# Performance work log

Measured on AMD Instinct MI355X. Metric: run time of the kernel, lower is better.

## Reference

```python
import jax, jax.numpy as jnp
import numpy as np

B, F, H, E = 16, 128, 144, 24   # batch, frames, num_harmonies, embedding
C0, C1 = 12, 12                 # harmony component dims (root, quality)


def setup_inputs() -> dict:
    key = jax.random.key(0)
    ks = jax.random.split(key, 7)
    note_embedding_seq = jax.random.normal(ks[0], (B, F, E), jnp.float32)
    # one-hot harmony vectors: concat(one_hot(root), one_hot(quality))
    idx = np.arange(H)
    hv = np.zeros((H, E), np.float32)
    hv[idx, idx // C1] = 1.0
    hv[idx, C0 + idx % C1] = 1.0
    harmony_vector = jnp.asarray(np.broadcast_to(hv, (B, H, E)).copy())
    s = 1.0 / np.sqrt(E)
    W0 = jax.random.uniform(ks[1], (C0, C0), jnp.float32, -s, s)
    b0 = jax.random.uniform(ks[2], (C0,), jnp.float32, -s, s)
    W1 = jax.random.uniform(ks[3], (C1, C1), jnp.float32, -s, s)
    b1 = jax.random.uniform(ks[4], (C1,), jnp.float32, -s, s)
    Wc = jax.random.uniform(ks[5], (E, E), jnp.float32, -s, s)
    bc = jax.random.uniform(ks[6], (E,), jnp.float32, -s, s)
    return {"note_embedding_seq": note_embedding_seq, "harmony_vector": harmony_vector,
            "W0": W0, "b0": b0, "W1": W1, "b1": b1, "Wc": Wc, "bc": bc}


def reference(note_embedding_seq, harmony_vector, W0, b0, W1, b1, Wc, bc):
    # HarmonyEncoder: per-component linear then combined linear
    h0 = harmony_vector[..., :C0] @ W0.T + b0
    h1 = harmony_vector[..., C0:] @ W1.T + b1
    q = jnp.concatenate([h0, h1], axis=-1) @ Wc.T + bc          # [B,H,E]

    # Per-segment attention. keys == values, so both the attention logits and
    # the value dot-products reduce to d[b,h,l] = q . k_l.  For segment [s,e]:
    #   score = sum_{l=s..e} softmax_seg(scale*d_l) * d_l
    # which is computed exactly for all segments via cumulative sums.
    scale = 1.0 / jnp.sqrt(jnp.float32(E))
    d = jnp.einsum('bhe,ble->bhl', q, note_embedding_seq)        # [B,H,F]
    m = jnp.max(d * scale, axis=-1, keepdims=True)               # global max: cancels in ratio
    p = jnp.exp(d * scale - m)                                   # [B,H,F]
    num = jnp.cumsum(p * d, axis=-1)                             # [B,H,F]
    den = jnp.cumsum(p, axis=-1)
    num0 = jnp.pad(num, ((0, 0), (0, 0), (1, 0)))[..., :F]       # cumsum up to s-1
    den0 = jnp.pad(den, ((0, 0), (0, 0), (1, 0)))[..., :F]
    dn = num[:, :, None, :] - num0[:, :, :, None]                # [B,H,s,e]
    dd = den[:, :, None, :] - den0[:, :, :, None]
    valid = jnp.triu(jnp.ones((F, F), bool))                     # e >= s
    score = jnp.where(valid, dn / jnp.where(valid, dd, 1.0), 0.0)
    return jnp.transpose(score, (0, 2, 3, 1))                    # [B,F,F,H]
```

## Files before the change

kernel.cpp:

```cpp
#include <hip/hip_runtime.h>
#include <hip/hip_bf16.h>

#define BB 16
#define FF 128
#define HH 144
#define EE 24
#define C0C 12

typedef float v4f __attribute__((ext_vector_type(4)));

#define TABLE_ELEMS (BB * (FF + 1) * HH)

__device__ __forceinline__ float fastdiv(float n, float d) {
    float r = __builtin_amdgcn_rcpf(d);
    r = fmaf(fmaf(-d, r, 1.0f), r, r);
    return n * r;
}

__global__ __launch_bounds__(256) void seg_pre(
    const float* __restrict__ note,
    const float* __restrict__ hv,
    const float* __restrict__ W0,
    const float* __restrict__ b0,
    const float* __restrict__ W1,
    const float* __restrict__ b1,
    const float* __restrict__ Wc,
    const float* __restrict__ bc,
    float* __restrict__ num_t,
    float* __restrict__ den_t,
    float* __restrict__ out)
{
    const int blk = blockIdx.x;
    const int tid = threadIdx.x;

    __shared__ float s_note[FF * EE];
    __shared__ float s_hcat[16][EE];
    __shared__ float s_q[16][EE];
    __shared__ float s_p[FF][16];
    __shared__ float s_pd[FF][16];
    __shared__ float s_pm[16][16];
    __shared__ float s_m[16];

    if (blk >= 144) {
        const int z = blk - 144;
        const int x = z & 7;
        const int t = z >> 3;
        const int b = 2 * x + (t >= 64);
        const int sp = (t >= 64) ? t - 64 : t;
        float* out_b = out + (size_t)b * (FF * FF * HH);

        v4f* r1 = reinterpret_cast<v4f*>(out_b + (size_t)sp * FF * HH);
        const int n1 = sp * (HH / 4);
        for (int c = tid; c < n1; c += 256) r1[c] = (v4f)(0.f);

        v4f* r2 = reinterpret_cast<v4f*>(out_b + (size_t)(127 - sp) * FF * HH);
        const int n2 = (127 - sp) * (HH / 4);
        for (int c = tid; c < n2; c += 256) r2[c] = (v4f)(0.f);
        return;
    }

    const int x = blk & 7;
    const int t = blk >> 3;
    const int b = 2 * x + (t >= 9);
    const int tile = (t >= 9) ? t - 9 : t;
    const int h0 = tile * 16;

    const float* nb_ = note + (size_t)b * FF * EE;
    for (int k = tid; k < FF * EE / 4; k += 256)
        reinterpret_cast<v4f*>(s_note)[k] = reinterpret_cast<const v4f*>(nb_)[k];

    for (int idx = tid; idx < 16 * EE; idx += 256) {
        const int hl = idx / EE, e = idx - hl * EE;
        const float* hvb = hv + ((size_t)b * HH + h0 + hl) * EE;
        float acc;
        if (e < C0C) {
            acc = b0[e];
            #pragma unroll
            for (int j = 0; j < C0C; ++j) acc += W0[e * C0C + j] * hvb[j];
        } else {
            const int e1 = e - C0C;
            acc = b1[e1];
            #pragma unroll
            for (int j = 0; j < C0C; ++j) acc += W1[e1 * C0C + j] * hvb[C0C + j];
        }
        s_hcat[hl][e] = acc;
    }
    __syncthreads();
    for (int idx = tid; idx < 16 * EE; idx += 256) {
        const int hl = idx / EE, e = idx - hl * EE;
        float acc = bc[e];
        #pragma unroll
        for (int j = 0; j < EE; ++j) acc += Wc[e * EE + j] * s_hcat[hl][j];
        s_q[hl][e] = acc;
    }
    __syncthreads();

    const int hl = tid & 15;
    const int f0 = tid >> 4;
    const float scale = 0.20412414523193150818f;

    float dv[8];
    float pmax = -3.4e38f;
    #pragma unroll
    for (int k = 0; k < 8; ++k) {
        const int f = f0 + (k << 4);
        float acc = 0.f;
        #pragma unroll
        for (int e = 0; e < EE; ++e) acc += s_q[hl][e] * s_note[f * EE + e];
        dv[k] = acc;
        pmax = fmaxf(pmax, acc);
    }
    s_pm[f0][hl] = pmax * scale;
    __syncthreads();
    if (tid < 16) {
        float m = s_pm[0][tid];
        #pragma unroll
        for (int r = 1; r < 16; ++r) m = fmaxf(m, s_pm[r][tid]);
        s_m[tid] = m;
    }
    __syncthreads();
    const float m = s_m[hl];

    #pragma unroll
    for (int k = 0; k < 8; ++k) {
        const int f = f0 + (k << 4);
        const float p = __expf(dv[k] * scale - m);
        s_p[f][hl] = p;
        s_pd[f][hl] = p * dv[k];
    }
    __syncthreads();

    for (int off = 1; off < FF; off <<= 1) {
        float tp[8], tpd[8];
        #pragma unroll
        for (int k = 0; k < 8; ++k) {
            const int f = f0 + (k << 4);
            tp[k] = (f >= off) ? s_p[f - off][hl] : 0.f;
            tpd[k] = (f >= off) ? s_pd[f - off][hl] : 0.f;
        }
        __syncthreads();
        #pragma unroll
        for (int k = 0; k < 8; ++k) {
            const int f = f0 + (k << 4);
            if (f >= off) { s_p[f][hl] += tp[k]; s_pd[f][hl] += tpd[k]; }
        }
        __syncthreads();
    }

    const size_t base = (size_t)b * (FF + 1) * HH + h0;
    for (int idx4 = tid; idx4 < 512; idx4 += 256) {
        const int f = idx4 >> 2;
        const int hh = (idx4 & 3) * 4;
        *reinterpret_cast<v4f*>(num_t + base + (size_t)(f + 1) * HH + hh) =
            *reinterpret_cast<const v4f*>(&s_pd[f][hh]);
        *reinterpret_cast<v4f*>(den_t + base + (size_t)(f + 1) * HH + hh) =
            *reinterpret_cast<const v4f*>(&s_p[f][hh]);
    }
    if (tid < 16) {
        num_t[base + tid] = 0.f;
        den_t[base + tid] = 0.f;
    }
}

__device__ __forceinline__ void k2_row_half(
    const float* __restrict__ nb, const float* __restrict__ db,
    float* __restrict__ out_b, int s, int tid, int half)
{
    float* ob = out_b + (size_t)s * (FF * HH);

    if (tid < 252) {
        const int r = tid / 36;
        const int hq = tid - r * 36;
        const int h = hq * 4;

        const v4f n0 = *reinterpret_cast<const v4f*>(nb + (size_t)s * HH + h);
        const v4f d0 = *reinterpret_cast<const v4f*>(db + (size_t)s * HH + h);

        const int e0 = s + r + 7 * half;
        const float* pn = nb + (size_t)(e0 + 1) * HH + h;
        const float* pd_ = db + (size_t)(e0 + 1) * HH + h;
        float* po = ob + (size_t)e0 * HH + h;

        #pragma unroll 2
        for (int e = e0; e < FF; e += 14) {
            const v4f n1 = *reinterpret_cast<const v4f*>(pn);
            const v4f d1 = *reinterpret_cast<const v4f*>(pd_);
            v4f val;
            val.x = fastdiv(n1.x - n0.x, d1.x - d0.x);
            val.y = fastdiv(n1.y - n0.y, d1.y - d0.y);
            val.z = fastdiv(n1.z - n0.z, d1.z - d0.z);
            val.w = fastdiv(n1.w - n0.w, d1.w - d0.w);
            *reinterpret_cast<v4f*>(po) = val;
            pn += 14 * HH;
            pd_ += 14 * HH;
            po += 14 * HH;
        }
    }
}

__global__ __launch_bounds__(256) void seg_k2(
    const float* __restrict__ num_t,
    const float* __restrict__ den_t,
    float* __restrict__ out)
{
    const int blk = blockIdx.x;
    const int x = blk & 7;
    const int t = blk >> 3;
    const int b = 2 * x + (t >= 128);
    const int j = t & 127;
    const int sp = j >> 1;
    const int half = j & 1;
    const int tid = threadIdx.x;

    const float* nb = num_t + (size_t)b * (FF + 1) * HH;
    const float* db = den_t + (size_t)b * (FF + 1) * HH;
    float* out_b = out + (size_t)b * (FF * FF * HH);

    k2_row_half(nb, db, out_b, sp, tid, half);
    k2_row_half(nb, db, out_b, 127 - sp, tid, half);
}

extern "C" void kernel_launch(void* const* d_in, const int* in_sizes, int n_in,
                              void* d_out, int out_size, void* d_ws, size_t ws_size,
                              hipStream_t stream) {
    const float* note = (const float*)d_in[0];
    const float* hv   = (const float*)d_in[1];
    const float* W0   = (const float*)d_in[2];
    const float* b0   = (const float*)d_in[3];
    const float* W1   = (const float*)d_in[4];
    const float* b1   = (const float*)d_in[5];
    const float* Wc   = (const float*)d_in[6];
    const float* bc   = (const float*)d_in[7];
    float* out = (float*)d_out;

    float* num_t = (float*)d_ws;
    float* den_t = num_t + TABLE_ELEMS;

    seg_pre<<<144 + 1024, 256, 0, stream>>>(note, hv, W0, b0, W1, b1, Wc, bc,
                                            num_t, den_t, out);
    seg_k2<<<BB * FF, 256, 0, stream>>>(num_t, den_t, out);
}
```

Before: 34.18 us.

## Tile seg_k2 by harmony slices and stage prefix tables in shared memory

Rewrites the second kernel so each block owns a 16-harmony slice of one batch and eight start rows, staging that slice of the num/den prefix tables in LDS once and then computing segment ratios from LDS. Previously each block handled two full start rows across all 144 harmonies, reading prefix tables directly from global memory. The new layout cuts redundant global/L2 reads of the tables. In exchange each output write is a 64-byte chunk per row rather than a 576-byte contiguous row, which may hurt write coalescing, and the grid grows to 2304 blocks.

```diff
diff --git a/kernel.cpp b/kernel.cpp
--- a/kernel.cpp
+++ b/kernel.cpp
@@ -162,42 +162,6 @@
     }
 }
 
-__device__ __forceinline__ void k2_row_half(
-    const float* __restrict__ nb, const float* __restrict__ db,
-    float* __restrict__ out_b, int s, int tid, int half)
-{
-    float* ob = out_b + (size_t)s * (FF * HH);
-
-    if (tid < 252) {
-        const int r = tid / 36;
-        const int hq = tid - r * 36;
-        const int h = hq * 4;
-
-        const v4f n0 = *reinterpret_cast<const v4f*>(nb + (size_t)s * HH + h);
-        const v4f d0 = *reinterpret_cast<const v4f*>(db + (size_t)s * HH + h);
-
-        const int e0 = s + r + 7 * half;
-        const float* pn = nb + (size_t)(e0 + 1) * HH + h;
-        const float* pd_ = db + (size_t)(e0 + 1) * HH + h;
-        float* po = ob + (size_t)e0 * HH + h;
-
-        #pragma unroll 2
-        for (int e = e0; e < FF; e += 14) {
-            const v4f n1 = *reinterpret_cast<const v4f*>(pn);
-            const v4f d1 = *reinterpret_cast<const v4f*>(pd_);
-            v4f val;
-            val.x = fastdiv(n1.x - n0.x, d1.x - d0.x);
-            val.y = fastdiv(n1.y - n0.y, d1.y - d0.y);
-            val.z = fastdiv(n1.z - n0.z, d1.z - d0.z);
-            val.w = fastdiv(n1.w - n0.w, d1.w - d0.w);
-            *reinterpret_cast<v4f*>(po) = val;
-            pn += 14 * HH;
-            pd_ += 14 * HH;
-            po += 14 * HH;
-        }
-    }
-}
-
 __global__ __launch_bounds__(256) void seg_k2(
     const float* __restrict__ num_t,
     const float* __restrict__ den_t,
@@ -205,19 +169,60 @@
 {
     const int blk = blockIdx.x;
     const int x = blk & 7;
-    const int t = blk >> 3;
-    const int b = 2 * x + (t >= 128);
-    const int j = t & 127;
-    const int sp = j >> 1;
-    const int half = j & 1;
+    const int v = blk >> 3;
+    const int b = 2 * x + (v >= 144);
+    const int w = (v >= 144) ? v - 144 : v;
+    const int hs = w >> 4;
+    const int g = w & 15;
+    const int h0 = hs * 16;
     const int tid = threadIdx.x;
 
-    const float* nb = num_t + (size_t)b * (FF + 1) * HH;
-    const float* db = den_t + (size_t)b * (FF + 1) * HH;
-    float* out_b = out + (size_t)b * (FF * FF * HH);
-
-    k2_row_half(nb, db, out_b, sp, tid, half);
-    k2_row_half(nb, db, out_b, 127 - sp, tid, half);
+    __shared__ float s_n[FF + 1][16];
+    __shared__ float s_d[FF + 1][16];
+
+    const float* nb = num_t + (size_t)b * (FF + 1) * HH + h0;
+    const float* db = den_t + (size_t)b * (FF + 1) * HH + h0;
+
+    for (int i = tid; i < (FF + 1) * 4; i += 256) {
+        const int f = i >> 2;
+        const int c = (i & 3) * 4;
+        *reinterpret_cast<v4f*>(&s_n[f][c]) =
+            *reinterpret_cast<const v4f*>(nb + (size_t)f * HH + c);
+        *reinterpret_cast<v4f*>(&s_d[f][c]) =
+            *reinterpret_cast<const v4f*>(db + (size_t)f * HH + c);
+    }
+    __syncthreads();
+
+    const int c4 = (tid & 3) * 4;
+    const int r = tid >> 2;
+    float* out_bh = out + (size_t)b * (FF * FF * HH) + h0 + c4;
+
+    #pragma unroll
+    for (int pp = 0; pp < 4; ++pp) {
+        const int s_lo = g * 4 + pp;
+        #pragma unroll
+        for (int side = 0; side < 2; ++side) {
+            const int s = side ? 127 - s_lo : s_lo;
+            const v4f n0 = *reinterpret_cast<const v4f*>(&s_n[s][c4]);
+            const v4f d0 = *reinterpret_cast<const v4f*>(&s_d[s][c4]);
+            float* os = out_bh + (size_t)s * (FF * HH);
+
+            int e = s + r;
+            #pragma unroll
+            for (int k = 0; k < 2; ++k, e += 64) {
+                if (e < FF) {
+                    const v4f n1 = *reinterpret_cast<const v4f*>(&s_n[e + 1][c4]);
+                    const v4f d1 = *reinterpret_cast<const v4f*>(&s_d[e + 1][c4]);
+                    v4f val;
+                    val.x = fastdiv(n1.x - n0.x, d1.x - d0.x);
+                    val.y = fastdiv(n1.y - n0.y, d1.y - d0.y);
+                    val.z = fastdiv(n1.z - n0.z, d1.z - d0.z);
+                    val.w = fastdiv(n1.w - n0.w, d1.w - d0.w);
+                    *reinterpret_cast<v4f*>(os + (size_t)e * HH) = val;
+                }
+            }
+        }
+    }
 }
 
 extern "C" void kernel_launch(void* const* d_in, const int* in_sizes, int n_in,
@@ -238,5 +243,5 @@
 
     seg_pre<<<144 + 1024, 256, 0, stream>>>(note, hv, W0, b0, W1, b1, Wc, bc,
                                             num_t, den_t, out);
-    seg_k2<<<BB * FF, 256, 0, stream>>>(num_t, den_t, out);
-}
+    seg_k2<<<2304, 256, 0, stream>>>(num_t, den_t, out);
+}
```

Measured after the change: 35.86 us. 1.05x slower.

## Interleave num/den tables and process two start rows per loaded end row

Applied to the files above, without the earlier changes.

The cumulative numerator and denominator tables are now stored interleaved, so one set of vector loads fetches both values for two harmonies. Each block of the segment kernel now handles a pair of adjacent start rows (a, a+1) and reuses each loaded end-row entry for both outputs. This halves table reads per output and drops the separate num/den streams. In exchange there is a data-dependent branch in the inner loop and a different row-to-block assignment that may affect load balance.

```diff
diff --git a/kernel.cpp b/kernel.cpp
--- a/kernel.cpp
+++ b/kernel.cpp
@@ -9,7 +9,7 @@
 
 typedef float v4f __attribute__((ext_vector_type(4)));
 
-#define TABLE_ELEMS (BB * (FF + 1) * HH)
+#define PK_ELEMS (BB * (FF + 1) * HH * 2)
 
 __device__ __forceinline__ float fastdiv(float n, float d) {
     float r = __builtin_amdgcn_rcpf(d);
@@ -26,8 +26,7 @@
     const float* __restrict__ b1,
     const float* __restrict__ Wc,
     const float* __restrict__ bc,
-    float* __restrict__ num_t,
-    float* __restrict__ den_t,
+    float* __restrict__ pk,
     float* __restrict__ out)
 {
     const int blk = blockIdx.x;
@@ -147,77 +146,77 @@
         __syncthreads();
     }
 
-    const size_t base = (size_t)b * (FF + 1) * HH + h0;
-    for (int idx4 = tid; idx4 < 512; idx4 += 256) {
-        const int f = idx4 >> 2;
-        const int hh = (idx4 & 3) * 4;
-        *reinterpret_cast<v4f*>(num_t + base + (size_t)(f + 1) * HH + hh) =
-            *reinterpret_cast<const v4f*>(&s_pd[f][hh]);
-        *reinterpret_cast<v4f*>(den_t + base + (size_t)(f + 1) * HH + hh) =
-            *reinterpret_cast<const v4f*>(&s_p[f][hh]);
-    }
-    if (tid < 16) {
-        num_t[base + tid] = 0.f;
-        den_t[base + tid] = 0.f;
-    }
-}
-
-__device__ __forceinline__ void k2_row_half(
-    const float* __restrict__ nb, const float* __restrict__ db,
-    float* __restrict__ out_b, int s, int tid, int half)
-{
-    float* ob = out_b + (size_t)s * (FF * HH);
-
-    if (tid < 252) {
-        const int r = tid / 36;
-        const int hq = tid - r * 36;
-        const int h = hq * 4;
-
-        const v4f n0 = *reinterpret_cast<const v4f*>(nb + (size_t)s * HH + h);
-        const v4f d0 = *reinterpret_cast<const v4f*>(db + (size_t)s * HH + h);
-
-        const int e0 = s + r + 7 * half;
-        const float* pn = nb + (size_t)(e0 + 1) * HH + h;
-        const float* pd_ = db + (size_t)(e0 + 1) * HH + h;
-        float* po = ob + (size_t)e0 * HH + h;
-
-        #pragma unroll 2
-        for (int e = e0; e < FF; e += 14) {
-            const v4f n1 = *reinterpret_cast<const v4f*>(pn);
-            const v4f d1 = *reinterpret_cast<const v4f*>(pd_);
-            v4f val;
-            val.x = fastdiv(n1.x - n0.x, d1.x - d0.x);
-            val.y = fastdiv(n1.y - n0.y, d1.y - d0.y);
-            val.z = fastdiv(n1.z - n0.z, d1.z - d0.z);
-            val.w = fastdiv(n1.w - n0.w, d1.w - d0.w);
-            *reinterpret_cast<v4f*>(po) = val;
-            pn += 14 * HH;
-            pd_ += 14 * HH;
-            po += 14 * HH;
-        }
+    float* pkb = pk + ((size_t)b * (FF + 1) * HH + h0) * 2;
+    for (int idx4 = tid; idx4 < 1024; idx4 += 256) {
+        const int f = idx4 >> 3;
+        const int hh = (idx4 & 7) * 2;
+        v4f val;
+        val.x = s_pd[f][hh];
+        val.y = s_p[f][hh];
+        val.z = s_pd[f][hh + 1];
+        val.w = s_p[f][hh + 1];
+        *reinterpret_cast<v4f*>(pkb + ((size_t)(f + 1) * HH + hh) * 2) = val;
+    }
+    if (tid < 8) {
+        *reinterpret_cast<v4f*>(pkb + tid * 4) = (v4f)(0.f);
     }
 }
 
 __global__ __launch_bounds__(256) void seg_k2(
-    const float* __restrict__ num_t,
-    const float* __restrict__ den_t,
+    const float* __restrict__ pk,
     float* __restrict__ out)
 {
     const int blk = blockIdx.x;
     const int x = blk & 7;
-    const int t = blk >> 3;
-    const int b = 2 * x + (t >= 128);
-    const int j = t & 127;
-    const int sp = j >> 1;
-    const int half = j & 1;
+    const int rest = blk >> 3;
+    const int bsel = rest >> 7;
+    const int r2 = rest & 127;
+    const int g = r2 >> 2;
+    const int q = r2 & 3;
+    const int b = 2 * x + bsel;
     const int tid = threadIdx.x;
-
-    const float* nb = num_t + (size_t)b * (FF + 1) * HH;
-    const float* db = den_t + (size_t)b * (FF + 1) * HH;
+    if (tid >= 252) return;
+
+    const int r = tid / 36;
+    const int hq = tid - r * 36;
+    const int h = hq * 4;
+
+    const float* tb = pk + (size_t)b * (FF + 1) * (HH * 2);
     float* out_b = out + (size_t)b * (FF * FF * HH);
 
-    k2_row_half(nb, db, out_b, sp, tid, half);
-    k2_row_half(nb, db, out_b, 127 - sp, tid, half);
+    #pragma unroll
+    for (int side = 0; side < 2; ++side) {
+        const int a = side ? 126 - 2 * g : 2 * g;
+
+        const v4f za_lo = *reinterpret_cast<const v4f*>(tb + ((size_t)a * HH + h) * 2);
+        const v4f za_hi = *reinterpret_cast<const v4f*>(tb + ((size_t)a * HH + h) * 2 + 4);
+        const v4f zb_lo = *reinterpret_cast<const v4f*>(tb + ((size_t)(a + 1) * HH + h) * 2);
+        const v4f zb_hi = *reinterpret_cast<const v4f*>(tb + ((size_t)(a + 1) * HH + h) * 2 + 4);
+
+        float* ob0 = out_b + (size_t)a * (FF * HH) + h;
+        float* ob1 = out_b + (size_t)(a + 1) * (FF * HH) + h;
+
+        for (int e = a + r + 7 * q; e < FF; e += 28) {
+            const v4f t_lo = *reinterpret_cast<const v4f*>(tb + ((size_t)(e + 1) * HH + h) * 2);
+            const v4f t_hi = *reinterpret_cast<const v4f*>(tb + ((size_t)(e + 1) * HH + h) * 2 + 4);
+
+            v4f v0;
+            v0.x = fastdiv(t_lo.x - za_lo.x, t_lo.y - za_lo.y);
+            v0.y = fastdiv(t_lo.z - za_lo.z, t_lo.w - za_lo.w);
+            v0.z = fastdiv(t_hi.x - za_hi.x, t_hi.y - za_hi.y);
+            v0.w = fastdiv(t_hi.z - za_hi.z, t_hi.w - za_hi.w);
+            *reinterpret_cast<v4f*>(ob0 + (size_t)e * HH) = v0;
+
+            if (e > a) {
+                v4f v1;
+                v1.x = fastdiv(t_lo.x - zb_lo.x, t_lo.y - zb_lo.y);
+                v1.y = fastdiv(t_lo.z - zb_lo.z, t_lo.w - zb_lo.w);
+                v1.z = fastdiv(t_hi.x - zb_hi.x, t_hi.y - zb_hi.y);
+                v1.w = fastdiv(t_hi.z - zb_hi.z, t_hi.w - zb_hi.w);
+                *reinterpret_cast<v4f*>(ob1 + (size_t)e * HH) = v1;
+            }
+        }
+    }
 }
 
 extern "C" void kernel_launch(void* const* d_in, const int* in_sizes, int n_in,
@@ -233,10 +232,9 @@
     const float* bc   = (const float*)d_in[7];
     float* out = (float*)d_out;
 
-    float* num_t = (float*)d_ws;
-    float* den_t = num_t + TABLE_ELEMS;
+    float* pk = (float*)d_ws;
 
     seg_pre<<<144 + 1024, 256, 0, stream>>>(note, hv, W0, b0, W1, b1, Wc, bc,
-                                            num_t, den_t, out);
-    seg_k2<<<BB * FF, 256, 0, stream>>>(num_t, den_t, out);
-}
+                                            pk, out);
+    seg_k2<<<2048, 256, 0, stream>>>(pk, out);
+}
```

New measurement: 33.99 us. Within noise of the previous version (-0.6%).
